# Kernel tuning notes

Hardware: AMD Instinct MI355X
Metric: run time of the kernel (lower is better)

The kernel has to match this reference:

```python
import jax, jax.numpy as jnp
import numpy as np

B, L, D = 4, 8192, 1024
H, HD = 16, 64  # num_heads, head_dim (qkv_features = H*HD = 1024)
EPS = 1e-06


def elu_feature_map(x):
    return jax.nn.elu(x) + 1.0


def setup_inputs() -> dict:
    key = jax.random.key(0)
    ks = jax.random.split(key, 9)
    # xavier-uniform-ish scales
    def xav(k, shape, fan_in, fan_out):
        lim = jnp.sqrt(6.0 / (fan_in + fan_out))
        return jax.random.uniform(k, shape, jnp.float32, -lim, lim)
    x = jax.random.normal(ks[0], (B, L, D), jnp.float32)
    Wq = xav(ks[1], (D, H, HD), D, H * HD)
    Wk = xav(ks[2], (D, H, HD), D, H * HD)
    Wv = xav(ks[3], (D, H, HD), D, H * HD)
    Wo = xav(ks[4], (H, HD, D), H * HD, D)
    bq = jax.random.normal(ks[5], (H, HD), jnp.float32) * 1e-06
    bk = jax.random.normal(ks[6], (H, HD), jnp.float32) * 1e-06
    bv = jax.random.normal(ks[7], (H, HD), jnp.float32) * 1e-06
    bo = jax.random.normal(ks[8], (D,), jnp.float32) * 1e-06
    return {"x": x, "Wq": Wq, "bq": bq, "Wk": Wk, "bk": bk,
            "Wv": Wv, "bv": bv, "Wo": Wo, "bo": bo}


def reference(x, Wq, bq, Wk, bk, Wv, bv, Wo, bo):
    # QKV projections (DenseGeneral axis=-1 -> (H, HD))
    q = jnp.einsum('nld,dhk->nlhk', x, Wq) + bq  # [B,L,H,HD]
    k = jnp.einsum('nld,dhk->nlhk', x, Wk) + bk
    v = jnp.einsum('nld,dhk->nlhk', x, Wv) + bv
    # Kernelized linear attention
    qf = elu_feature_map(q)
    kf = elu_feature_map(k)
    kv = jnp.einsum('nshd,nshm->nhmd', kf, v)          # [B,H,HD,HD]
    z = 1.0 / (jnp.einsum('nlhd,nhd->nlh', qf, jnp.sum(kf, axis=1)) + EPS)
    y = jnp.einsum('nlhd,nhmd,nlh->nlhm', qf, kv, z)   # [B,L,H,HD]
    # Output projection (DenseGeneral over (-2,-1))
    out = jnp.einsum('nlhm,hmd->nld', y, Wo) + bo      # [B,L,D]
    return out
```

## Files before the change

### kernel.cpp

```cpp
#include <hip/hip_runtime.h>
#include <stdint.h>

typedef unsigned short u16;
typedef __attribute__((ext_vector_type(8))) short bf16x8;
typedef __attribute__((ext_vector_type(8))) unsigned short u16x8;
typedef __attribute__((ext_vector_type(4))) unsigned short u16x4;
typedef __attribute__((ext_vector_type(4))) float f32x4;

#define AS1 __attribute__((address_space(1)))
#define AS3 __attribute__((address_space(3)))

__device__ __forceinline__ u16 f32_to_bf16(float f) {
  unsigned int u = __builtin_bit_cast(unsigned int, f);
  u += 0x7FFFu + ((u >> 16) & 1u);
  return (u16)(u >> 16);
}
__device__ __forceinline__ float bf16_to_f32(u16 s) {
  return __builtin_bit_cast(float, (unsigned int)s << 16);
}
__device__ __forceinline__ void g2lds16(const void* g, void* l) {
  __builtin_amdgcn_global_load_lds((const AS1 void*)g, (AS3 void*)l, 16, 0, 0);
}

__global__ __launch_bounds__(256) void cvt_x(const float* __restrict__ x, u16* __restrict__ xb) {
  size_t base = ((size_t)blockIdx.x * 256 + threadIdx.x) * 8;
  const size_t stride = (size_t)2048 * 256 * 8;
  #pragma unroll
  for (int it = 0; it < 8; ++it, base += stride) {
    float4 a = *(const float4*)(x + base);
    float4 b = *(const float4*)(x + base + 4);
    u16x8 o;
    o[0]=f32_to_bf16(a.x); o[1]=f32_to_bf16(a.y); o[2]=f32_to_bf16(a.z); o[3]=f32_to_bf16(a.w);
    o[4]=f32_to_bf16(b.x); o[5]=f32_to_bf16(b.y); o[6]=f32_to_bf16(b.z); o[7]=f32_to_bf16(b.w);
    *(u16x8*)(xb + base) = o;
  }
}

__global__ void cvt_wt(const float* __restrict__ Wq, const float* __restrict__ Wk,
                       const float* __restrict__ Wv, const float* __restrict__ Wo,
                       u16* __restrict__ WT) {
  __shared__ float tile[32][33];
  const float* W = blockIdx.z==0 ? Wq : blockIdx.z==1 ? Wk : blockIdx.z==2 ? Wv : Wo;
  int n0 = blockIdx.x*32, k0 = blockIdx.y*32;
  int tx = threadIdx.x, ty = threadIdx.y;
  for (int r = ty; r < 32; r += 8)
    tile[r][tx] = W[(size_t)(k0+r)*1024 + n0 + tx];
  __syncthreads();
  u16* out = WT + (size_t)blockIdx.z*1024*1024;
  for (int r = ty; r < 32; r += 8)
    out[(size_t)(n0+r)*1024 + k0 + tx] = f32_to_bf16(tile[tx][r]);
}

__global__ __launch_bounds__(256) void init_vvT(u16* __restrict__ vvT) {
  int idx = blockIdx.x*256 + threadIdx.x;
  int p = idx >> 14, rem = idx & 16383;
  int row = 64 + (rem >> 10), col8 = (rem & 1023) * 8;
  u16 v = (row == 64) ? (u16)0x3F80 : (u16)0;
  u16x8 o = {v,v,v,v,v,v,v,v};
  *(u16x8*)(vvT + ((size_t)p*80 + row)*8192 + col8) = o;
}

template<int MODE>
__global__ __launch_bounds__(512) void gemm8(const u16* __restrict__ A, const u16* __restrict__ WT,
    const float* __restrict__ bq, const float* __restrict__ bk, const float* __restrict__ bv,
    u16* __restrict__ qf, u16* __restrict__ kfT, u16* __restrict__ vvT,
    float* __restrict__ fout) {
  extern __shared__ u16 lds[];
  const int z = (MODE==0) ? blockIdx.y : 3;
  const u16* Bt = WT + (size_t)z*1048576;
  int bid = blockIdx.x;
  int swz = (bid & 7)*64 + (bid >> 3);
  int rb = swz >> 2, cb = swz & 3;
  const int gm0 = rb*256, gn0 = cb*256;
  const int t = threadIdx.x, w = t>>6, l = t&63;
  const int wm = w>>2, wn = w&3;
  const int lrow = l & 15, lks = l >> 4;
  const int csw = (l&7) ^ (l>>3);
  const u16* aBase = A  + (size_t)(gm0 + w*8 + (l>>3))*1024 + csw*8;
  const u16* bBase = Bt + (size_t)(gn0 + w*8 + (l>>3))*1024 + csw*8;

  f32x4 acc[2][2][4][2];
  const f32x4 vzero = {0.f,0.f,0.f,0.f};
  #pragma unroll
  for (int a0=0;a0<2;++a0)
    #pragma unroll
    for (int b0i=0;b0i<2;++b0i)
      #pragma unroll
      for (int c0=0;c0<4;++c0)
        #pragma unroll
        for (int d0=0;d0<2;++d0) acc[a0][b0i][c0][d0] = vzero;

  #pragma unroll
  for (int half=0; half<2; ++half)
    #pragma unroll
    for (int j=0;j<2;++j) {
      g2lds16(aBase + (half*128 + j*64)*1024, (char*)lds + half*16384 + j*8192 + w*1024);
      g2lds16(bBase + (half*128 + j*64)*1024, (char*)lds + 65536 + half*16384 + j*8192 + w*1024);
    }
  asm volatile("s_waitcnt vmcnt(0)" ::: "memory");
  __builtin_amdgcn_s_barrier();
  asm volatile("" ::: "memory");

  #pragma unroll
  for (int kt = 0; kt < 16; ++kt) {
    const int buf = kt & 1;
    const char* Ab = (const char*)lds + buf*32768;
    const char* Bb = (const char*)lds + 65536 + buf*32768;
    char* An = (char*)lds + (buf^1)*32768;
    char* Bn = (char*)lds + 65536 + (buf^1)*32768;
    const u16* aSrc = aBase + (size_t)(kt+1)*64;
    const u16* bSrc = bBase + (size_t)(kt+1)*64;
    const bool pf = (kt < 15);

    bf16x8 af0[4][2], af1[4][2];
    bf16x8 b0[2][2], b1[2][2];

    #define LD_A(DST,MH)                                                     \
      _Pragma("unroll")                                                      \
      for (int mi=0;mi<4;++mi) {                                             \
        int row = (MH)*128 + wm*64 + mi*16 + lrow;                           \
        _Pragma("unroll")                                                    \
        for (int kx=0;kx<2;++kx)                                             \
          DST[mi][kx] = *(const bf16x8*)(Ab + row*128 + (((kx*4+lks) ^ (row&7))<<4)); \
      }
    #define LD_B(DST,NH)                                                     \
      _Pragma("unroll")                                                      \
      for (int ni=0;ni<2;++ni) {                                             \
        int row = (NH)*128 + wn*32 + ni*16 + lrow;                           \
        _Pragma("unroll")                                                    \
        for (int kx=0;kx<2;++kx)                                             \
          DST[ni][kx] = *(const bf16x8*)(Bb + row*128 + (((kx*4+lks) ^ (row&7))<<4)); \
      }
    #define MFMA16(MH,NH,AF,BF)                                              \
      __builtin_amdgcn_s_setprio(1);                                         \
      _Pragma("unroll")                                                      \
      for (int mi=0;mi<4;++mi)                                               \
        _Pragma("unroll")                                                    \
        for (int ni=0;ni<2;++ni) {                                           \
          acc[MH][NH][mi][ni] = __builtin_amdgcn_mfma_f32_16x16x32_bf16(AF[mi][0], BF[ni][0], acc[MH][NH][mi][ni], 0,0,0); \
          acc[MH][NH][mi][ni] = __builtin_amdgcn_mfma_f32_16x16x32_bf16(AF[mi][1], BF[ni][1], acc[MH][NH][mi][ni], 0,0,0); \
        }                                                                    \
      __builtin_amdgcn_s_setprio(0);                                         \
      __builtin_amdgcn_s_barrier();                                          \
      asm volatile("" ::: "memory");

    LD_A(af0, 0); LD_B(b0, 0);
    if (pf) { g2lds16(aSrc, An + w*1024); g2lds16(aSrc + 64*1024, An + 8192 + w*1024); }
    __builtin_amdgcn_s_barrier();
    asm volatile("" ::: "memory");
    LD_B(b1, 1);
    MFMA16(0, 0, af0, b0);

    if (pf) { g2lds16(bSrc, Bn + w*1024); g2lds16(bSrc + 64*1024, Bn + 8192 + w*1024); }
    if (pf) { asm volatile("s_waitcnt vmcnt(4)" ::: "memory"); }
    else    { asm volatile("s_waitcnt vmcnt(0)" ::: "memory"); }
    __builtin_amdgcn_s_barrier();
    asm volatile("" ::: "memory");
    LD_A(af1, 1);
    MFMA16(0, 1, af0, b1);

    if (pf) { g2lds16(bSrc + 128*1024, Bn + 16384 + w*1024); g2lds16(bSrc + 192*1024, Bn + 24576 + w*1024); }
    __builtin_amdgcn_s_barrier();
    asm volatile("" ::: "memory");
    MFMA16(1, 1, af1, b1);

    if (pf) { g2lds16(aSrc + 128*1024, An + 16384 + w*1024); g2lds16(aSrc + 192*1024, An + 24576 + w*1024); }
    if (pf) { asm volatile("s_waitcnt vmcnt(2)" ::: "memory"); }
    __builtin_amdgcn_s_barrier();
    asm volatile("" ::: "memory");
    MFMA16(1, 0, af1, b0);

    #undef LD_A
    #undef LD_B
    #undef MFMA16
  }

  if (MODE == 0) {
    const float* bias = z==0 ? bq : (z==1 ? bk : bv);
    const bool feat = (z < 2);
    if (z == 0) {
      #pragma unroll
      for (int mh=0;mh<2;++mh)
        #pragma unroll
        for (int nh=0;nh<2;++nh)
          #pragma unroll
          for (int mi=0;mi<4;++mi)
            #pragma unroll
            for (int ni=0;ni<2;++ni) {
              int n = gn0 + nh*128 + wn*32 + ni*16 + lrow;
              float bn = bias[n];
              int h = n>>6, hd = n&63;
              int mbase = gm0 + mh*128 + wm*64 + mi*16 + (lks<<2);
              #pragma unroll
              for (int r=0;r<4;++r) {
                int m = mbase + r;
                float val = acc[mh][nh][mi][ni][r] + bn;
                val = val>0.f ? val+1.f : __expf(val);
                qf[((size_t)((m>>13)*16 + h)*8192 + (m&8191))*64 + hd] = f32_to_bf16(val);
              }
            }
    } else {
      u16* outp = (z==1) ? kfT : vvT;
      const size_t prow = (z==1) ? 64 : 80;
      #pragma unroll
      for (int mh=0;mh<2;++mh)
        #pragma unroll
        for (int nh=0;nh<2;++nh)
          #pragma unroll
          for (int mi=0;mi<4;++mi)
            #pragma unroll
            for (int ni=0;ni<2;++ni) {
              int n = gn0 + nh*128 + wn*32 + ni*16 + lrow;
              float bn = bias[n];
              int h = n>>6, hd = n&63;
              int mbase = gm0 + mh*128 + wm*64 + mi*16 + (lks<<2);
              int b_ = mbase >> 13, s = mbase & 8191;
              u16x4 pk;
              #pragma unroll
              for (int r=0;r<4;++r) {
                float val = acc[mh][nh][mi][ni][r] + bn;
                if (feat) val = val>0.f ? val+1.f : __expf(val);
                pk[r] = f32_to_bf16(val);
              }
              *(u16x4*)(outp + ((size_t)(b_*16 + h)*prow + hd)*8192 + s) = pk;
            }
    }
  } else {
    #pragma unroll
    for (int mh=0;mh<2;++mh)
      #pragma unroll
      for (int nh=0;nh<2;++nh)
        #pragma unroll
        for (int mi=0;mi<4;++mi)
          #pragma unroll
          for (int ni=0;ni<2;++ni) {
            int n = gn0 + nh*128 + wn*32 + ni*16 + lrow;
            float bn = bq[n];
            int mbase = gm0 + mh*128 + wm*64 + mi*16 + (lks<<2);
            #pragma unroll
            for (int r=0;r<4;++r) {
              int m = mbase + r;
              fout[(size_t)m*1024 + n] = acc[mh][nh][mi][ni][r] + bn;
            }
          }
  }
}

__global__ __launch_bounds__(256) void kv_mfma(const u16* __restrict__ kfT, const u16* __restrict__ vvT,
                                               float* __restrict__ pkv) {
  __shared__ __align__(16) u16 lA[80*256];
  __shared__ __align__(16) u16 lB[64*256];
  const int p = blockIdx.x, c = blockIdx.y;
  const int t = threadIdx.x, w = t>>6, l = t&63;
  const int srow = t >> 5;
  const int csw = (t&31) ^ ((t>>5)&7);
  const u16* aRow = vvT + ((size_t)p*80 + srow)*8192 + (size_t)c*512 + csw*8;
  const u16* bRow = kfT + ((size_t)p*64 + srow)*8192 + (size_t)c*512 + csw*8;

  f32x4 acc5[5];
  const f32x4 vzero = {0.f,0.f,0.f,0.f};
  #pragma unroll
  for (int mi=0;mi<5;++mi) acc5[mi] = vzero;

  for (int sub = 0; sub < 2; ++sub) {
    const size_t so = (size_t)sub*256;
    #pragma unroll
    for (int i=0;i<10;++i)
      g2lds16(aRow + (size_t)i*8*8192 + so, (char*)lA + i*4096 + t*16);
    #pragma unroll
    for (int i=0;i<8;++i)
      g2lds16(bRow + (size_t)i*8*8192 + so, (char*)lB + i*4096 + t*16);
    asm volatile("s_waitcnt vmcnt(0)" ::: "memory");
    __builtin_amdgcn_s_barrier();
    asm volatile("" ::: "memory");
    #pragma unroll
    for (int ks=0;ks<8;++ks) {
      const int brow = w*16 + (l&15);
      const int slot = ks*4 + (l>>4);
      bf16x8 bfr = *(const bf16x8*)((const char*)lB + brow*512 + ((slot ^ (brow&7))<<4));
      #pragma unroll
      for (int mi=0;mi<5;++mi) {
        const int arow = mi*16 + (l&15);
        bf16x8 afr = *(const bf16x8*)((const char*)lA + arow*512 + ((slot ^ (arow&7))<<4));
        acc5[mi] = __builtin_amdgcn_mfma_f32_16x16x32_bf16(afr, bfr, acc5[mi], 0,0,0);
      }
    }
    __builtin_amdgcn_s_barrier();
    asm volatile("" ::: "memory");
  }

  float* po = pkv + ((size_t)p*16 + c)*5120;
  #pragma unroll
  for (int mi=0;mi<5;++mi)
    #pragma unroll
    for (int r=0;r<4;++r)
      po[(mi*16 + (l>>4)*4 + r)*64 + w*16 + (l&15)] = acc5[mi][r];
}

__global__ __launch_bounds__(256) void kv_reduce(const float* __restrict__ pkv, u16* __restrict__ bkv) {
  int p = blockIdx.x, t = threadIdx.x;
  for (int i = t; i < 5120; i += 256) {
    float s = 0.f;
    for (int c = 0; c < 16; ++c) s += pkv[((size_t)p*16 + c)*5120 + i];
    bkv[(size_t)p*5120 + i] = f32_to_bf16(s);
  }
}

__global__ __launch_bounds__(256) void y_gemm(const u16* __restrict__ qf, const u16* __restrict__ bkv,
                                              u16* __restrict__ y) {
  __shared__ __align__(16) u16 As[256*64];
  __shared__ __align__(16) u16 Bs[80*64];
  int p = blockIdx.x, rb = blockIdx.y;
  int t = threadIdx.x, wave = t >> 6, lane = t & 63;
  const u16* aslab = qf + ((size_t)p*8192 + (size_t)rb*256)*64;
  for (int i = t*8; i < 5120; i += 2048)
    *(int4*)&Bs[i] = *(const int4*)&bkv[(size_t)p*5120 + i];
  #pragma unroll
  for (int it = 0; it < 8; ++it)
    g2lds16(aslab + it*2048 + t*8, (char*)As + it*4096 + wave*1024);
  __syncthreads();
  const f32x4 vzero = {0.f,0.f,0.f,0.f};
  f32x4 acc[4][5];
  #pragma unroll
  for (int mi=0;mi<4;++mi)
    #pragma unroll
    for (int ni=0;ni<5;++ni) acc[mi][ni] = vzero;
  #pragma unroll
  for (int kk = 0; kk < 64; kk += 32) {
    bf16x8 af[4], bfr[5];
    #pragma unroll
    for (int mi=0;mi<4;++mi)
      af[mi] = *(const bf16x8*)&As[(wave*64 + mi*16 + (lane&15))*64 + kk + (lane>>4)*8];
    #pragma unroll
    for (int ni=0;ni<5;++ni)
      bfr[ni] = *(const bf16x8*)&Bs[(ni*16 + (lane&15))*64 + kk + (lane>>4)*8];
    #pragma unroll
    for (int mi=0;mi<4;++mi)
      #pragma unroll
      for (int ni=0;ni<5;++ni)
        acc[mi][ni] = __builtin_amdgcn_mfma_f32_16x16x32_bf16(af[mi], bfr[ni], acc[mi][ni], 0, 0, 0);
  }
  int b_ = p >> 4, h = p & 15;
  #pragma unroll
  for (int mi=0;mi<4;++mi) {
    #pragma unroll
    for (int r=0;r<4;++r) {
      float den = __shfl(acc[mi][4][r], lane & 48);
      float zf = 1.0f / (den + 1e-6f);
      int lq = rb*256 + wave*64 + mi*16 + ((lane>>4)<<2) + r;
      size_t rowbase = ((size_t)(b_*8192 + lq)*16 + h)*64;
      #pragma unroll
      for (int ni=0;ni<4;++ni)
        y[rowbase + ni*16 + (lane&15)] = f32_to_bf16(acc[mi][ni][r] * zf);
    }
  }
}

extern "C" void kernel_launch(void* const* d_in, const int* in_sizes, int n_in,
                              void* d_out, int out_size, void* d_ws, size_t ws_size,
                              hipStream_t stream) {
  const float* x  = (const float*)d_in[0];
  const float* Wq = (const float*)d_in[1];
  const float* bq = (const float*)d_in[2];
  const float* Wk = (const float*)d_in[3];
  const float* bk = (const float*)d_in[4];
  const float* Wv = (const float*)d_in[5];
  const float* bv = (const float*)d_in[6];
  const float* Wo = (const float*)d_in[7];
  const float* bo = (const float*)d_in[8];
  float* out = (float*)d_out;
  char* ws = (char*)d_ws;

  u16*  xb  = (u16*)(ws);
  u16*  WT  = (u16*)(ws + 67108864);
  u16*  qf  = (u16*)(ws + 75497472);
  u16*  kfT = (u16*)(ws + 142606336);
  u16*  vvT = (u16*)(ws + 209715200);
  u16*  bkv = (u16*)(ws + 293601280);
  float* pkv = (float*)(ws);
  u16*  yb  = xb;

  auto kq = gemm8<0>; auto ko = gemm8<1>;
  hipFuncSetAttribute((const void*)kq, hipFuncAttributeMaxDynamicSharedMemorySize, 131072);
  hipFuncSetAttribute((const void*)ko, hipFuncAttributeMaxDynamicSharedMemorySize, 131072);

  cvt_x<<<2048, 256, 0, stream>>>(x, xb);
  cvt_wt<<<dim3(32,32,4), dim3(32,8), 0, stream>>>(Wq, Wk, Wv, Wo, WT);
  init_vvT<<<4096, 256, 0, stream>>>(vvT);
  gemm8<0><<<dim3(512,3), 512, 131072, stream>>>(xb, WT, bq, bk, bv, qf, kfT, vvT, nullptr);
  kv_mfma<<<dim3(64,16), 256, 0, stream>>>(kfT, vvT, pkv);
  kv_reduce<<<64, 256, 0, stream>>>(pkv, bkv);
  y_gemm<<<dim3(64,32), 256, 0, stream>>>(qf, bkv, yb);
  gemm8<1><<<dim3(512,1), 512, 131072, stream>>>(yb, WT, bo, nullptr, nullptr, nullptr, nullptr, nullptr, out);
}
```

Measured before the change: 427.0 us.

## Make GEMM blocks persistent over multiple output tiles with cross-job prefetch

The QKV and output GEMMs now launch 256 blocks, one per CU, and each block loops over several 256x256 output tiles (6 in QKV mode, 2 in output mode) that share the same A row block. The first K-slice of the next job's B tile is prefetched during the last k-step of the current job, so the pipeline does not drain between tiles. The goal is to remove tail and launch imbalance and to reuse the A rows from L2 across tiles. The cost is that each epilogue store now serialises with the following job's compute, and the single-wave grid has no other blocks to hide latency.

Measured after the change: 830.9 us. 1.95x slower.

```diff
diff --git a/kernel.cpp b/kernel.cpp
--- a/kernel.cpp
+++ b/kernel.cpp
@@ -66,119 +66,181 @@
     u16* __restrict__ qf, u16* __restrict__ kfT, u16* __restrict__ vvT,
     float* __restrict__ fout) {
   extern __shared__ u16 lds[];
-  const int z = (MODE==0) ? blockIdx.y : 3;
-  const u16* Bt = WT + (size_t)z*1048576;
+  const int NJOBS = (MODE==0) ? 6 : 2;
   int bid = blockIdx.x;
-  int swz = (bid & 7)*64 + (bid >> 3);
-  int rb = swz >> 2, cb = swz & 3;
-  const int gm0 = rb*256, gn0 = cb*256;
+  int swz = (bid & 7)*32 + (bid >> 3);
+  int rb = swz >> 1, cbp = swz & 1;
+  const int gm0 = rb*256;
   const int t = threadIdx.x, w = t>>6, l = t&63;
   const int wm = w>>2, wn = w&3;
   const int lrow = l & 15, lks = l >> 4;
   const int csw = (l&7) ^ (l>>3);
-  const u16* aBase = A  + (size_t)(gm0 + w*8 + (l>>3))*1024 + csw*8;
-  const u16* bBase = Bt + (size_t)(gn0 + w*8 + (l>>3))*1024 + csw*8;
-
-  f32x4 acc[2][2][4][2];
-  const f32x4 vzero = {0.f,0.f,0.f,0.f};
-  #pragma unroll
-  for (int a0=0;a0<2;++a0)
-    #pragma unroll
-    for (int b0i=0;b0i<2;++b0i)
-      #pragma unroll
-      for (int c0=0;c0<4;++c0)
-        #pragma unroll
-        for (int d0=0;d0<2;++d0) acc[a0][b0i][c0][d0] = vzero;
-
-  #pragma unroll
-  for (int half=0; half<2; ++half)
-    #pragma unroll
-    for (int j=0;j<2;++j) {
-      g2lds16(aBase + (half*128 + j*64)*1024, (char*)lds + half*16384 + j*8192 + w*1024);
-      g2lds16(bBase + (half*128 + j*64)*1024, (char*)lds + 65536 + half*16384 + j*8192 + w*1024);
-    }
-  asm volatile("s_waitcnt vmcnt(0)" ::: "memory");
+  const u16* aBase = A + (size_t)(gm0 + w*8 + (l>>3))*1024 + csw*8;
+  const size_t bOff = (size_t)(w*8 + (l>>3))*1024 + csw*8;
+
+  #define JOB_Z(J)   ((MODE==0) ? ((J)>>1) : 3)
+  #define JOB_CB(J)  ((MODE==0) ? (cbp*2 + ((J)&1)) : (cbp*2 + (J)))
+  #define JOB_B(J)   (WT + (size_t)JOB_Z(J)*1048576 + (size_t)(JOB_CB(J)*256)*1024 + bOff)
+
+  {
+    const u16* b0Base = JOB_B(0);
+    g2lds16(aBase,             (char*)lds + w*1024);
+    g2lds16(aBase + 64*1024,   (char*)lds + 8192 + w*1024);
+    g2lds16(b0Base,            (char*)lds + 65536 + w*1024);
+    g2lds16(b0Base + 64*1024,  (char*)lds + 65536 + 8192 + w*1024);
+    g2lds16(aBase + 128*1024,  (char*)lds + 16384 + w*1024);
+    g2lds16(aBase + 192*1024,  (char*)lds + 24576 + w*1024);
+    g2lds16(b0Base + 128*1024, (char*)lds + 65536 + 16384 + w*1024);
+    g2lds16(b0Base + 192*1024, (char*)lds + 65536 + 24576 + w*1024);
+  }
+  asm volatile("s_waitcnt vmcnt(4)" ::: "memory");
   __builtin_amdgcn_s_barrier();
   asm volatile("" ::: "memory");
 
-  #pragma unroll
-  for (int kt = 0; kt < 16; ++kt) {
-    const int buf = kt & 1;
-    const char* Ab = (const char*)lds + buf*32768;
-    const char* Bb = (const char*)lds + 65536 + buf*32768;
-    char* An = (char*)lds + (buf^1)*32768;
-    char* Bn = (char*)lds + 65536 + (buf^1)*32768;
-    const u16* aSrc = aBase + (size_t)(kt+1)*64;
-    const u16* bSrc = bBase + (size_t)(kt+1)*64;
-    const bool pf = (kt < 15);
-
-    bf16x8 af0[4][2], af1[4][2];
-    bf16x8 b0[2][2], b1[2][2];
-
-    #define LD_A(DST,MH)                                                     \
-      _Pragma("unroll")                                                      \
-      for (int mi=0;mi<4;++mi) {                                             \
-        int row = (MH)*128 + wm*64 + mi*16 + lrow;                           \
-        _Pragma("unroll")                                                    \
-        for (int kx=0;kx<2;++kx)                                             \
-          DST[mi][kx] = *(const bf16x8*)(Ab + row*128 + (((kx*4+lks) ^ (row&7))<<4)); \
+  for (int j = 0; j < NJOBS; ++j) {
+    const u16* bBase = JOB_B(j);
+    const u16* bNext = (j+1 < NJOBS) ? JOB_B(j+1) : bBase;
+    const int z = JOB_Z(j);
+    const int gn0 = JOB_CB(j)*256;
+
+    f32x4 acc[2][2][4][2];
+    const f32x4 vzero = {0.f,0.f,0.f,0.f};
+    #pragma unroll
+    for (int a0=0;a0<2;++a0)
+      #pragma unroll
+      for (int b0i=0;b0i<2;++b0i)
+        #pragma unroll
+        for (int c0=0;c0<4;++c0)
+          #pragma unroll
+          for (int d0=0;d0<2;++d0) acc[a0][b0i][c0][d0] = vzero;
+
+    #pragma unroll
+    for (int kt = 0; kt < 16; ++kt) {
+      const int buf = kt & 1;
+      const char* Ab = (const char*)lds + buf*32768;
+      const char* Bb = (const char*)lds + 65536 + buf*32768;
+      char* An = (char*)lds + (buf^1)*32768;
+      char* Bn = (char*)lds + 65536 + (buf^1)*32768;
+      const bool lastkt = (kt == 15);
+      const bool pf = !lastkt || (j+1 < NJOBS);
+      const u16* aSrc = lastkt ? aBase : aBase + (size_t)(kt+1)*64;
+      const u16* bSrc = lastkt ? bNext : bBase + (size_t)(kt+1)*64;
+
+      bf16x8 af0[4][2], af1[4][2];
+      bf16x8 b0[2][2], b1[2][2];
+
+      #define LD_A(DST,MH)                                                     \
+        _Pragma("unroll")                                                      \
+        for (int mi=0;mi<4;++mi) {                                             \
+          int row = (MH)*128 + wm*64 + mi*16 + lrow;                           \
+          _Pragma("unroll")                                                    \
+          for (int kx=0;kx<2;++kx)                                             \
+            DST[mi][kx] = *(const bf16x8*)(Ab + row*128 + (((kx*4+lks) ^ (row&7))<<4)); \
+        }
+      #define LD_B(DST,NH)                                                     \
+        _Pragma("unroll")                                                      \
+        for (int ni=0;ni<2;++ni) {                                             \
+          int row = (NH)*128 + wn*32 + ni*16 + lrow;                           \
+          _Pragma("unroll")                                                    \
+          for (int kx=0;kx<2;++kx)                                             \
+            DST[ni][kx] = *(const bf16x8*)(Bb + row*128 + (((kx*4+lks) ^ (row&7))<<4)); \
+        }
+      #define MFMA16(MH,NH,AF,BF)                                              \
+        __builtin_amdgcn_s_setprio(1);                                         \
+        _Pragma("unroll")                                                      \
+        for (int mi=0;mi<4;++mi)                                               \
+          _Pragma("unroll")                                                    \
+          for (int ni=0;ni<2;++ni) {                                           \
+            acc[MH][NH][mi][ni] = __builtin_amdgcn_mfma_f32_16x16x32_bf16(AF[mi][0], BF[ni][0], acc[MH][NH][mi][ni], 0,0,0); \
+            acc[MH][NH][mi][ni] = __builtin_amdgcn_mfma_f32_16x16x32_bf16(AF[mi][1], BF[ni][1], acc[MH][NH][mi][ni], 0,0,0); \
+          }                                                                    \
+        __builtin_amdgcn_s_setprio(0);                                         \
+        __builtin_amdgcn_s_barrier();                                          \
+        asm volatile("" ::: "memory");
+
+      LD_A(af0, 0); LD_B(b0, 0);
+      if (pf) { g2lds16(aSrc, An + w*1024); g2lds16(aSrc + 64*1024, An + 8192 + w*1024); }
+      if (j == 0 && kt == 0) { asm volatile("s_waitcnt vmcnt(2)" ::: "memory"); }
+      __builtin_amdgcn_s_barrier();
+      asm volatile("" ::: "memory");
+      LD_B(b1, 1);
+      MFMA16(0, 0, af0, b0);
+
+      if (pf) { g2lds16(bSrc, Bn + w*1024); g2lds16(bSrc + 64*1024, Bn + 8192 + w*1024); }
+      if (pf) { asm volatile("s_waitcnt vmcnt(4)" ::: "memory"); }
+      else    { asm volatile("s_waitcnt vmcnt(0)" ::: "memory"); }
+      __builtin_amdgcn_s_barrier();
+      asm volatile("" ::: "memory");
+      LD_A(af1, 1);
+      MFMA16(0, 1, af0, b1);
+
+      if (pf) { g2lds16(bSrc + 128*1024, Bn + 16384 + w*1024); g2lds16(bSrc + 192*1024, Bn + 24576 + w*1024); }
+      __builtin_amdgcn_s_barrier();
+      asm volatile("" ::: "memory");
+      MFMA16(1, 1, af1, b1);
+
+      if (pf) { g2lds16(aSrc + 128*1024, An + 16384 + w*1024); g2lds16(aSrc + 192*1024, An + 24576 + w*1024); }
+      if (pf) { asm volatile("s_waitcnt vmcnt(2)" ::: "memory"); }
+      __builtin_amdgcn_s_barrier();
+      asm volatile("" ::: "memory");
+      MFMA16(1, 0, af1, b0);
+
+      #undef LD_A
+      #undef LD_B
+      #undef MFMA16
+    }
+
+    if (MODE == 0) {
+      const float* bias = z==0 ? bq : (z==1 ? bk : bv);
+      const bool feat = (z < 2);
+      if (z == 0) {
+        #pragma unroll
+        for (int mh=0;mh<2;++mh)
+          #pragma unroll
+          for (int nh=0;nh<2;++nh)
+            #pragma unroll
+            for (int mi=0;mi<4;++mi)
+              #pragma unroll
+              for (int ni=0;ni<2;++ni) {
+                int n = gn0 + nh*128 + wn*32 + ni*16 + lrow;
+                float bn = bias[n];
+                int h = n>>6, hd = n&63;
+                int mbase = gm0 + mh*128 + wm*64 + mi*16 + (lks<<2);
+                #pragma unroll
+                for (int r=0;r<4;++r) {
+                  int m = mbase + r;
+                  float val = acc[mh][nh][mi][ni][r] + bn;
+                  val = val>0.f ? val+1.f : __expf(val);
+                  qf[((size_t)((m>>13)*16 + h)*8192 + (m&8191))*64 + hd] = f32_to_bf16(val);
+                }
+              }
+      } else {
+        u16* outp = (z==1) ? kfT : vvT;
+        const size_t prow = (z==1) ? 64 : 80;
+        #pragma unroll
+        for (int mh=0;mh<2;++mh)
+          #pragma unroll
+          for (int nh=0;nh<2;++nh)
+            #pragma unroll
+            for (int mi=0;mi<4;++mi)
+              #pragma unroll
+              for (int ni=0;ni<2;++ni) {
+                int n = gn0 + nh*128 + wn*32 + ni*16 + lrow;
+                float bn = bias[n];
+                int h = n>>6, hd = n&63;
+                int mbase = gm0 + mh*128 + wm*64 + mi*16 + (lks<<2);
+                int b_ = mbase >> 13, s = mbase & 8191;
+                u16x4 pk;
+                #pragma unroll
+                for (int r=0;r<4;++r) {
+                  float val = acc[mh][nh][mi][ni][r] + bn;
+                  if (feat) val = val>0.f ? val+1.f : __expf(val);
+                  pk[r] = f32_to_bf16(val);
+                }
+                *(u16x4*)(outp + ((size_t)(b_*16 + h)*prow + hd)*8192 + s) = pk;
+              }
       }
-    #define LD_B(DST,NH)                                                     \
-      _Pragma("unroll")                                                      \
-      for (int ni=0;ni<2;++ni) {                                             \
-        int row = (NH)*128 + wn*32 + ni*16 + lrow;                           \
-        _Pragma("unroll")                                                    \
-        for (int kx=0;kx<2;++kx)                                             \
-          DST[ni][kx] = *(const bf16x8*)(Bb + row*128 + (((kx*4+lks) ^ (row&7))<<4)); \
-      }
-    #define MFMA16(MH,NH,AF,BF)                                              \
-      __builtin_amdgcn_s_setprio(1);                                         \
-      _Pragma("unroll")                                                      \
-      for (int mi=0;mi<4;++mi)                                               \
-        _Pragma("unroll")                                                    \
-        for (int ni=0;ni<2;++ni) {                                           \
-          acc[MH][NH][mi][ni] = __builtin_amdgcn_mfma_f32_16x16x32_bf16(AF[mi][0], BF[ni][0], acc[MH][NH][mi][ni], 0,0,0); \
-          acc[MH][NH][mi][ni] = __builtin_amdgcn_mfma_f32_16x16x32_bf16(AF[mi][1], BF[ni][1], acc[MH][NH][mi][ni], 0,0,0); \
-        }                                                                    \
-      __builtin_amdgcn_s_setprio(0);                                         \
-      __builtin_amdgcn_s_barrier();                                          \
-      asm volatile("" ::: "memory");
-
-    LD_A(af0, 0); LD_B(b0, 0);
-    if (pf) { g2lds16(aSrc, An + w*1024); g2lds16(aSrc + 64*1024, An + 8192 + w*1024); }
-    __builtin_amdgcn_s_barrier();
-    asm volatile("" ::: "memory");
-    LD_B(b1, 1);
-    MFMA16(0, 0, af0, b0);
-
-    if (pf) { g2lds16(bSrc, Bn + w*1024); g2lds16(bSrc + 64*1024, Bn + 8192 + w*1024); }
-    if (pf) { asm volatile("s_waitcnt vmcnt(4)" ::: "memory"); }
-    else    { asm volatile("s_waitcnt vmcnt(0)" ::: "memory"); }
-    __builtin_amdgcn_s_barrier();
-    asm volatile("" ::: "memory");
-    LD_A(af1, 1);
-    MFMA16(0, 1, af0, b1);
-
-    if (pf) { g2lds16(bSrc + 128*1024, Bn + 16384 + w*1024); g2lds16(bSrc + 192*1024, Bn + 24576 + w*1024); }
-    __builtin_amdgcn_s_barrier();
-    asm volatile("" ::: "memory");
-    MFMA16(1, 1, af1, b1);
-
-    if (pf) { g2lds16(aSrc + 128*1024, An + 16384 + w*1024); g2lds16(aSrc + 192*1024, An + 24576 + w*1024); }
-    if (pf) { asm volatile("s_waitcnt vmcnt(2)" ::: "memory"); }
-    __builtin_amdgcn_s_barrier();
-    asm volatile("" ::: "memory");
-    MFMA16(1, 0, af1, b0);
-
-    #undef LD_A
-    #undef LD_B
-    #undef MFMA16
-  }
-
-  if (MODE == 0) {
-    const float* bias = z==0 ? bq : (z==1 ? bk : bv);
-    const bool feat = (z < 2);
-    if (z == 0) {
+    } else {
       #pragma unroll
       for (int mh=0;mh<2;++mh)
         #pragma unroll
@@ -188,62 +250,19 @@
             #pragma unroll
             for (int ni=0;ni<2;++ni) {
               int n = gn0 + nh*128 + wn*32 + ni*16 + lrow;
-              float bn = bias[n];
-              int h = n>>6, hd = n&63;
+              float bn = bq[n];
               int mbase = gm0 + mh*128 + wm*64 + mi*16 + (lks<<2);
               #pragma unroll
               for (int r=0;r<4;++r) {
                 int m = mbase + r;
-                float val = acc[mh][nh][mi][ni][r] + bn;
-                val = val>0.f ? val+1.f : __expf(val);
-                qf[((size_t)((m>>13)*16 + h)*8192 + (m&8191))*64 + hd] = f32_to_bf16(val);
+                fout[(size_t)m*1024 + n] = acc[mh][nh][mi][ni][r] + bn;
               }
             }
-    } else {
-      u16* outp = (z==1) ? kfT : vvT;
-      const size_t prow = (z==1) ? 64 : 80;
-      #pragma unroll
-      for (int mh=0;mh<2;++mh)
-        #pragma unroll
-        for (int nh=0;nh<2;++nh)
-          #pragma unroll
-          for (int mi=0;mi<4;++mi)
-            #pragma unroll
-            for (int ni=0;ni<2;++ni) {
-              int n = gn0 + nh*128 + wn*32 + ni*16 + lrow;
-              float bn = bias[n];
-              int h = n>>6, hd = n&63;
-              int mbase = gm0 + mh*128 + wm*64 + mi*16 + (lks<<2);
-              int b_ = mbase >> 13, s = mbase & 8191;
-              u16x4 pk;
-              #pragma unroll
-              for (int r=0;r<4;++r) {
-                float val = acc[mh][nh][mi][ni][r] + bn;
-                if (feat) val = val>0.f ? val+1.f : __expf(val);
-                pk[r] = f32_to_bf16(val);
-              }
-              *(u16x4*)(outp + ((size_t)(b_*16 + h)*prow + hd)*8192 + s) = pk;
-            }
     }
-  } else {
-    #pragma unroll
-    for (int mh=0;mh<2;++mh)
-      #pragma unroll
-      for (int nh=0;nh<2;++nh)
-        #pragma unroll
-        for (int mi=0;mi<4;++mi)
-          #pragma unroll
-          for (int ni=0;ni<2;++ni) {
-            int n = gn0 + nh*128 + wn*32 + ni*16 + lrow;
-            float bn = bq[n];
-            int mbase = gm0 + mh*128 + wm*64 + mi*16 + (lks<<2);
-            #pragma unroll
-            for (int r=0;r<4;++r) {
-              int m = mbase + r;
-              fout[(size_t)m*1024 + n] = acc[mh][nh][mi][ni][r] + bn;
-            }
-          }
-  }
+  }
+  #undef JOB_Z
+  #undef JOB_CB
+  #undef JOB_B
 }
 
 __global__ __launch_bounds__(256) void kv_mfma(const u16* __restrict__ kfT, const u16* __restrict__ vvT,
@@ -387,9 +406,9 @@
   cvt_x<<<2048, 256, 0, stream>>>(x, xb);
   cvt_wt<<<dim3(32,32,4), dim3(32,8), 0, stream>>>(Wq, Wk, Wv, Wo, WT);
   init_vvT<<<4096, 256, 0, stream>>>(vvT);
-  gemm8<0><<<dim3(512,3), 512, 131072, stream>>>(xb, WT, bq, bk, bv, qf, kfT, vvT, nullptr);
+  gemm8<0><<<256, 512, 131072, stream>>>(xb, WT, bq, bk, bv, qf, kfT, vvT, nullptr);
   kv_mfma<<<dim3(64,16), 256, 0, stream>>>(kfT, vvT, pkv);
   kv_reduce<<<64, 256, 0, stream>>>(pkv, bkv);
   y_gemm<<<dim3(64,32), 256, 0, stream>>>(qf, bkv, yb);
-  gemm8<1><<<dim3(512,1), 512, 131072, stream>>>(yb, WT, bo, nullptr, nullptr, nullptr, nullptr, nullptr, out);
-}
+  gemm8<1><<<256, 512, 131072, stream>>>(yb, WT, bo, nullptr, nullptr, nullptr, nullptr, nullptr, out);
+}
```
